# Kernel tuning notes

Measured on AMD Instinct MI355X. Metric: run time of the kernel, lower is better.

Reference implementation:

```python
import jax, jax.numpy as jnp
import numpy as np

TAU = 2.0      # LIF membrane time constant (spikingjelly LIFNode tau=2.0)
V_TH = 1.0     # default spikingjelly threshold
ALPHA = 2.0    # ATan surrogate default alpha

@jax.custom_vjp
def atan_spike(x):
    # Heaviside forward, ATan surrogate backward (spikingjelly surrogate.ATan)
    return (x >= 0.0).astype(x.dtype)

def _spike_fwd(x):
    return atan_spike(x), x

def _spike_bwd(x, g):
    sg = (ALPHA / 2.0) / (1.0 + (jnp.pi / 2.0 * ALPHA * x) ** 2)
    return (g * sg,)

atan_spike.defvjp(_spike_fwd, _spike_bwd)


def setup_inputs() -> dict:
    key = jax.random.key(0)
    ks = jax.random.split(key, 4)
    B, L, C, H, NL, K = 64, 96, 32, 256, 2, 3
    inputs = jax.random.normal(ks[0], (B, L, C), jnp.float32)
    w_enc = jax.random.normal(ks[1], (H, 1, K), jnp.float32) * (1.0 / np.sqrt(K))
    b_enc = jnp.zeros((H,), jnp.float32)
    w_rnn = jax.random.normal(ks[2], (NL, H, H), jnp.float32) * (1.0 / np.sqrt(H))
    b_rnn = jnp.zeros((NL, H), jnp.float32)
    return {"inputs": inputs, "w_enc": w_enc, "b_enc": b_enc,
            "w_rnn": w_rnn, "b_rnn": b_rnn}


def reference(inputs, w_enc, b_enc, w_rnn, b_rnn):
    B, L, C = inputs.shape
    H = w_enc.shape[0]
    NL = w_rnn.shape[0]
    # --- 'conv' spike encoder: per-channel temporal conv -> [B*C, H, L] ---
    x = inputs.transpose(0, 2, 1).reshape(B * C, 1, L)
    h = jax.lax.conv_general_dilated(x, w_enc, (1,), 'SAME',
                                     dimension_numbers=('NCH', 'OIH', 'NCH'))
    h = h + b_enc[None, :, None]
    h = h.transpose(2, 0, 1)  # [L, B*C, H] time-major for scan

    def step(v, x_t):
        s = x_t
        new_v = []
        for l in range(NL):  # fixed small layer loop
            cur = s @ w_rnn[l].T + b_rnn[l]            # Linear
            vl = v[l] + (cur - v[l]) / TAU             # leaky integrate
            s = atan_spike(vl - V_TH)                  # fire (surrogate grad)
            vl = vl * (1.0 - jax.lax.stop_gradient(s)) # hard reset, detach_reset
            new_v.append(vl)
        return tuple(new_v), (s, new_v[-1])

    v0 = tuple(jnp.zeros((B * C, H), inputs.dtype) for _ in range(NL))
    _, (spks, mems) = jax.lax.scan(step, v0, h)
    # spks: [L, B*C, H] -> [B, C*H, L]
    spks = spks.reshape(L, B, C * H).transpose(1, 2, 0)
    return spks.transpose(0, 2, 1), spks[:, :, -1]
```

## Files before the change

### kernel.cpp

```cpp
#include <hip/hip_runtime.h>
#include <hip/hip_bf16.h>
#include <stdint.h>


using floatx4 = __attribute__((ext_vector_type(4))) float;
using intx4   = __attribute__((ext_vector_type(4))) int;

__global__ void prep_kernel(const float* __restrict__ w_enc,
                            const float* __restrict__ b_enc,
                            const float* __restrict__ w_rnn,
                            const float* __restrict__ b_rnn,
                            double* __restrict__ Wd,
                            double* __restrict__ C0d,
                            signed char* __restrict__ Bw8)
{
    const int o = blockIdx.x;
    const int lane = threadIdx.x;
    const float4 w0v = *(const float4*)(w_rnn + (size_t)o * 256 + lane * 4);
    double a0 = 0.0, a1 = 0.0, a2 = 0.0, ab = 0.0;
#pragma unroll
    for (int e = 0; e < 4; ++e) {
        const int i = lane * 4 + e;
        const double wv = (double)(((const float*)&w0v)[e]);
        a0 += wv * (double)w_enc[i * 3 + 0];
        a1 += wv * (double)w_enc[i * 3 + 1];
        a2 += wv * (double)w_enc[i * 3 + 2];
        ab += wv * (double)b_enc[i];
    }
    for (int off = 32; off > 0; off >>= 1) {
        a0 += __shfl_down(a0, off, 64);
        a1 += __shfl_down(a1, off, 64);
        a2 += __shfl_down(a2, off, 64);
        ab += __shfl_down(ab, off, 64);
    }
    if (lane == 0) {
        Wd[o * 3 + 0] = a0;
        Wd[o * 3 + 1] = a1;
        Wd[o * 3 + 2] = a2;
        C0d[o] = ab + (double)b_rnn[o];
    }
    const float4 w1v = *(const float4*)(w_rnn + 65536 + (size_t)o * 256 + lane * 4);
    unsigned int pack[4] = {0u, 0u, 0u, 0u};
#pragma unroll
    for (int e = 0; e < 4; ++e) {
        float f = ((const float*)&w1v)[e];
        int q = __double2int_rn((double)f * 134217728.0);
        int d3 = ((q + 64) & 127) - 64;  q = (q - d3) >> 7;
        int d2 = ((q + 64) & 127) - 64;  q = (q - d2) >> 7;
        int d1 = ((q + 64) & 127) - 64;  q = (q - d1) >> 7;
        int d0 = q;
        pack[0] |= ((unsigned int)(d0 & 0xFF)) << (8 * e);
        pack[1] |= ((unsigned int)(d1 & 0xFF)) << (8 * e);
        pack[2] |= ((unsigned int)(d2 & 0xFF)) << (8 * e);
        pack[3] |= ((unsigned int)(d3 & 0xFF)) << (8 * e);
    }
#pragma unroll
    for (int l = 0; l < 4; ++l)
        *(unsigned int*)(Bw8 + ((size_t)o * 4 + l) * 256 + lane * 4) = pack[l];
}

__global__ void enc_kernel(const float* __restrict__ inputs,
                           const double* __restrict__ Wd,
                           const double* __restrict__ C0d,
                           unsigned char* __restrict__ s0b)
{
    const int n = blockIdx.x;
    const int tidx = threadIdx.x;
    const int b = n >> 5, c = n & 31;
    __shared__ float xr[98];
    if (tidx < 96)       xr[tidx + 1] = inputs[((size_t)b * 96 + tidx) * 32 + c];
    else if (tidx == 96) xr[0]  = 0.0f;
    else if (tidx == 97) xr[97] = 0.0f;
    __syncthreads();
    const double W0 = Wd[tidx * 3], W1 = Wd[tidx * 3 + 1], W2 = Wd[tidx * 3 + 2];
    const double c0 = C0d[tidx];
    const int wid = tidx >> 6, lane = tidx & 63;
    float v = 0.0f;
    for (int t = 0; t < 96; ++t) {
        float cur = (float)((double)xr[t] * W0 + (double)xr[t + 1] * W1 +
                            (double)xr[t + 2] * W2 + c0);
        float vv = v + (cur - v) * 0.5f;
        int sp = (vv - 1.0f) >= 0.0f;
        v = sp ? 0.0f : vv;
        unsigned long long bal = __ballot(sp);
        if ((lane & 15) == 0) {
            const int j = lane >> 4;
            *(unsigned short*)(s0b + ((size_t)t * 2048 + n) * 32 + 8 * j + 2 * wid)
                = (unsigned short)(bal >> (16 * j));
        }
    }
}

__global__ __launch_bounds__(256, 2) void rnn_kernel(
    const unsigned char* __restrict__ s0b,
    const signed char* __restrict__ Bw8,
    const float* __restrict__ b_rnn,
    float* __restrict__ out0,
    float* __restrict__ out1)
{
    const int tid  = threadIdx.x;
    const int wid  = tid >> 6, lane = tid & 63;
    const int m    = lane & 15, g = lane >> 4;
    const int job  = blockIdx.x * 4 + wid;
    const int rt   = job >> 4;
    const int nw   = rt * 16;
    const int o0   = (job & 15) * 16;

    intx4 bfrag[4][4];
#pragma unroll
    for (int l = 0; l < 4; ++l)
#pragma unroll
        for (int c = 0; c < 4; ++c)
            bfrag[l][c] = *(const intx4*)(Bw8 + ((size_t)(o0 + m) * 4 + l) * 256
                                               + c * 64 + g * 16);
    const float bias = b_rnn[256 + o0 + m];

    float* pr[4];
    int    row_r[4];
#pragma unroll
    for (int r = 0; r < 4; ++r) {
        const int row = nw + g * 4 + r;
        row_r[r] = row;
        pr[r] = out0 + ((size_t)(row >> 5) * 96) * 8192 + (size_t)(row & 31) * 256
                     + o0 + m;
    }

    const unsigned char* mp = s0b + ((size_t)(nw + m)) * 32 + 8 * g;
    uint2 m0 = *(const uint2*)(mp);
    uint2 m1 = *(const uint2*)(mp + 65536);

    floatx4 v = {0.f, 0.f, 0.f, 0.f};

    for (int t = 0; t < 96; ++t) {
        uint2 pa = m1;
        if (t < 94)
            m1 = *(const uint2*)(mp + (size_t)(t + 2) * 65536);

        unsigned int hw[4] = { m0.x & 0xFFFFu, m0.x >> 16,
                               m0.y & 0xFFFFu, m0.y >> 16 };
        intx4 af[4];
#pragma unroll
        for (int c = 0; c < 4; ++c) {
            unsigned int h = hw[c];
            intx4 a;
            a.x = (int)((( h        & 0xFu) * 0x00204081u) & 0x01010101u);
            a.y = (int)((((h >> 4)  & 0xFu) * 0x00204081u) & 0x01010101u);
            a.z = (int)((((h >> 8)  & 0xFu) * 0x00204081u) & 0x01010101u);
            a.w = (int)((((h >> 12) & 0xFu) * 0x00204081u) & 0x01010101u);
            af[c] = a;
        }

        intx4 acc0 = {0,0,0,0}, acc1 = {0,0,0,0}, acc2 = {0,0,0,0}, acc3 = {0,0,0,0};
#pragma unroll
        for (int c = 0; c < 4; ++c) {
            acc0 = __builtin_amdgcn_mfma_i32_16x16x64_i8(af[c], bfrag[0][c], acc0, 0, 0, 0);
            acc1 = __builtin_amdgcn_mfma_i32_16x16x64_i8(af[c], bfrag[1][c], acc1, 0, 0, 0);
            acc2 = __builtin_amdgcn_mfma_i32_16x16x64_i8(af[c], bfrag[2][c], acc2, 0, 0, 0);
            acc3 = __builtin_amdgcn_mfma_i32_16x16x64_i8(af[c], bfrag[3][c], acc3, 0, 0, 0);
        }

#pragma unroll
        for (int r = 0; r < 4; ++r) {
            int a01 = acc0[r] * 128 + acc1[r];
            int a23 = acc2[r] * 128 + acc3[r];
            double dd = (double)a01 * 16384.0 + (double)a23;
            float cur = (float)(dd * 7.450580596923828125e-9) + bias;
            float vv = v[r];
            vv = vv + (cur - vv) * 0.5f;
            float s = ((vv - 1.0f) >= 0.0f) ? 1.0f : 0.0f;
            v[r] = vv * (1.0f - s);
            pr[r][(size_t)t * 8192] = s;
            if (t == 95)
                out1[(size_t)row_r[r] * 256 + o0 + m] = s;
        }
        m0 = pa;
    }
}

extern "C" void kernel_launch(void* const* d_in, const int* in_sizes, int n_in,
                              void* d_out, int out_size, void* d_ws, size_t ws_size,
                              hipStream_t stream) {
    const float* inputs = (const float*)d_in[0];
    const float* w_enc  = (const float*)d_in[1];
    const float* b_enc  = (const float*)d_in[2];
    const float* w_rnn  = (const float*)d_in[3];
    const float* b_rnn  = (const float*)d_in[4];

    float* out0 = (float*)d_out;
    float* out1 = out0 + (size_t)64 * 96 * 8192;

    char* ws = (char*)d_ws;
    double*      Wd  = (double*)(ws);
    double*      C0d = (double*)(ws + 6144);
    signed char* Bw8 = (signed char*)(ws + 8192);
    unsigned char* s0b = (unsigned char*)(ws + 270336);

    prep_kernel<<<256, 64, 0, stream>>>(w_enc, b_enc, w_rnn, b_rnn, Wd, C0d, Bw8);
    enc_kernel<<<2048, 256, 0, stream>>>(inputs, Wd, C0d, s0b);
    rnn_kernel<<<512, 256, 0, stream>>>(s0b, Bw8, b_rnn, out0, out1);
}
```

Baseline: 262.2 us.

## Write layer-2 spikes as packed bits and expand to floats in separate kernel

The recurrent kernel no longer scatters strided float stores to the output. It packs each lane's four spikes into a nibble byte in a workspace buffer, and a new expand kernel then writes out0 and out1 as coalesced float4 stores. The MFMA operands are swapped so each lane holds four output rows of one batch row, the double-precision current reconstruction becomes float FMAs, and the guard on the prefetch is dropped by reading past the end of the padded buffer. The change costs an extra kernel launch and an intermediate pass through global memory, and the float reconstruction may round differently near the threshold.

```diff
diff --git a/kernel.cpp b/kernel.cpp
--- a/kernel.cpp
+++ b/kernel.cpp
@@ -95,8 +95,7 @@
     const unsigned char* __restrict__ s0b,
     const signed char* __restrict__ Bw8,
     const float* __restrict__ b_rnn,
-    float* __restrict__ out0,
-    float* __restrict__ out1)
+    unsigned char* __restrict__ s1b)
 {
     const int tid  = threadIdx.x;
     const int wid  = tid >> 6, lane = tid & 63;
@@ -104,7 +103,8 @@
     const int job  = blockIdx.x * 4 + wid;
     const int rt   = job >> 4;
     const int nw   = rt * 16;
-    const int o0   = (job & 15) * 16;
+    const int jo   = job & 15;
+    const int o0   = jo * 16;
 
     intx4 bfrag[4][4];
 #pragma unroll
@@ -113,17 +113,9 @@
         for (int c = 0; c < 4; ++c)
             bfrag[l][c] = *(const intx4*)(Bw8 + ((size_t)(o0 + m) * 4 + l) * 256
                                                + c * 64 + g * 16);
-    const float bias = b_rnn[256 + o0 + m];
-
-    float* pr[4];
-    int    row_r[4];
-#pragma unroll
-    for (int r = 0; r < 4; ++r) {
-        const int row = nw + g * 4 + r;
-        row_r[r] = row;
-        pr[r] = out0 + ((size_t)(row >> 5) * 96) * 8192 + (size_t)(row & 31) * 256
-                     + o0 + m;
-    }
+    const float4 biasv = *(const float4*)(b_rnn + 256 + o0 + g * 4);
+
+    unsigned char* sp_ptr = s1b + (size_t)jo * 8192 + (size_t)(nw + m) * 4 + g;
 
     const unsigned char* mp = s0b + ((size_t)(nw + m)) * 32 + 8 * g;
     uint2 m0 = *(const uint2*)(mp);
@@ -132,48 +124,76 @@
     floatx4 v = {0.f, 0.f, 0.f, 0.f};
 
     for (int t = 0; t < 96; ++t) {
-        uint2 pa = m1;
-        if (t < 94)
-            m1 = *(const uint2*)(mp + (size_t)(t + 2) * 65536);
-
-        unsigned int hw[4] = { m0.x & 0xFFFFu, m0.x >> 16,
-                               m0.y & 0xFFFFu, m0.y >> 16 };
-        intx4 af[4];
-#pragma unroll
-        for (int c = 0; c < 4; ++c) {
-            unsigned int h = hw[c];
-            intx4 a;
-            a.x = (int)((( h        & 0xFu) * 0x00204081u) & 0x01010101u);
-            a.y = (int)((((h >> 4)  & 0xFu) * 0x00204081u) & 0x01010101u);
-            a.z = (int)((((h >> 8)  & 0xFu) * 0x00204081u) & 0x01010101u);
-            a.w = (int)((((h >> 12) & 0xFu) * 0x00204081u) & 0x01010101u);
-            af[c] = a;
-        }
+        uint2 nxt = m1;
+        m1 = *(const uint2*)(mp + (size_t)(t + 2) * 65536);
 
         intx4 acc0 = {0,0,0,0}, acc1 = {0,0,0,0}, acc2 = {0,0,0,0}, acc3 = {0,0,0,0};
-#pragma unroll
-        for (int c = 0; c < 4; ++c) {
-            acc0 = __builtin_amdgcn_mfma_i32_16x16x64_i8(af[c], bfrag[0][c], acc0, 0, 0, 0);
-            acc1 = __builtin_amdgcn_mfma_i32_16x16x64_i8(af[c], bfrag[1][c], acc1, 0, 0, 0);
-            acc2 = __builtin_amdgcn_mfma_i32_16x16x64_i8(af[c], bfrag[2][c], acc2, 0, 0, 0);
-            acc3 = __builtin_amdgcn_mfma_i32_16x16x64_i8(af[c], bfrag[3][c], acc3, 0, 0, 0);
-        }
-
+        {
+            unsigned int hw_[4] = { m0.x & 0xFFFFu, m0.x >> 16,
+                                    m0.y & 0xFFFFu, m0.y >> 16 };
+#pragma unroll
+            for (int c = 0; c < 4; ++c) {
+                unsigned int h_ = hw_[c];
+                intx4 a_;
+                a_.x = (int)((( h_        & 0xFu) * 0x00204081u) & 0x01010101u);
+                a_.y = (int)((((h_ >> 4)  & 0xFu) * 0x00204081u) & 0x01010101u);
+                a_.z = (int)((((h_ >> 8)  & 0xFu) * 0x00204081u) & 0x01010101u);
+                a_.w = (int)((((h_ >> 12) & 0xFu) * 0x00204081u) & 0x01010101u);
+                acc0 = __builtin_amdgcn_mfma_i32_16x16x64_i8(bfrag[0][c], a_, acc0, 0, 0, 0);
+                acc1 = __builtin_amdgcn_mfma_i32_16x16x64_i8(bfrag[1][c], a_, acc1, 0, 0, 0);
+                acc2 = __builtin_amdgcn_mfma_i32_16x16x64_i8(bfrag[2][c], a_, acc2, 0, 0, 0);
+                acc3 = __builtin_amdgcn_mfma_i32_16x16x64_i8(bfrag[3][c], a_, acc3, 0, 0, 0);
+            }
+        }
+
+        unsigned int nib = 0u;
 #pragma unroll
         for (int r = 0; r < 4; ++r) {
             int a01 = acc0[r] * 128 + acc1[r];
             int a23 = acc2[r] * 128 + acc3[r];
-            double dd = (double)a01 * 16384.0 + (double)a23;
-            float cur = (float)(dd * 7.450580596923828125e-9) + bias;
+            float cur = fmaf((float)a01, 0x1p-13f, (float)a23 * 0x1p-27f)
+                        + ((const float*)&biasv)[r];
             float vv = v[r];
             vv = vv + (cur - vv) * 0.5f;
-            float s = ((vv - 1.0f) >= 0.0f) ? 1.0f : 0.0f;
-            v[r] = vv * (1.0f - s);
-            pr[r][(size_t)t * 8192] = s;
-            if (t == 95)
-                out1[(size_t)row_r[r] * 256 + o0 + m] = s;
-        }
-        m0 = pa;
+            bool sp = (vv - 1.0f) >= 0.0f;
+            nib |= sp ? (1u << r) : 0u;
+            v[r] = sp ? 0.0f : vv;
+        }
+        sp_ptr[(size_t)t * 131072] = (unsigned char)nib;
+        m0 = nxt;
+    }
+}
+
+__global__ void expand_kernel(const unsigned char* __restrict__ s1b,
+                              float* __restrict__ out0,
+                              float* __restrict__ out1)
+{
+    const unsigned int tid0 = blockIdx.x * 256u + threadIdx.x;
+#pragma unroll
+    for (int it = 0; it < 6; ++it) {
+        const unsigned int gi = tid0 + (unsigned int)it * 524288u;
+        const unsigned int bt = gi >> 9;
+        const unsigned int b  = bt / 96u;
+        const unsigned int t  = bt - b * 96u;
+        const unsigned int cc = (gi >> 4) & 31u;
+        const unsigned int k  = (gi * 4u) & 63u;
+        const unsigned int n  = b * 32u + cc;
+        const unsigned int quad = *(const unsigned int*)(s1b
+                + (size_t)t * 131072u + (size_t)(k >> 2) * 8192u + (size_t)n * 4u);
+        float* po = out0 + (size_t)gi * 16u;
+        const bool last = (t == 95u);
+        float* p1 = out1 + (size_t)b * 8192u + (size_t)cc * 256u + (size_t)k * 4u;
+#pragma unroll
+        for (int j = 0; j < 4; ++j) {
+            const unsigned int nib = (quad >> (8 * j)) & 0xFu;
+            float4 w;
+            w.x = (float)( nib        & 1u);
+            w.y = (float)((nib >> 1u) & 1u);
+            w.z = (float)((nib >> 2u) & 1u);
+            w.w = (float)((nib >> 3u) & 1u);
+            *(float4*)(po + 4 * j) = w;
+            if (last) *(float4*)(p1 + 4 * j) = w;
+        }
     }
 }
 
@@ -190,12 +210,14 @@
     float* out1 = out0 + (size_t)64 * 96 * 8192;
 
     char* ws = (char*)d_ws;
-    double*      Wd  = (double*)(ws);
-    double*      C0d = (double*)(ws + 6144);
-    signed char* Bw8 = (signed char*)(ws + 8192);
+    double*        Wd  = (double*)(ws);
+    double*        C0d = (double*)(ws + 6144);
+    signed char*   Bw8 = (signed char*)(ws + 8192);
     unsigned char* s0b = (unsigned char*)(ws + 270336);
+    unsigned char* s1b = s0b + (size_t)98 * 65536;
 
     prep_kernel<<<256, 64, 0, stream>>>(w_enc, b_enc, w_rnn, b_rnn, Wd, C0d, Bw8);
     enc_kernel<<<2048, 256, 0, stream>>>(inputs, Wd, C0d, s0b);
-    rnn_kernel<<<512, 256, 0, stream>>>(s0b, Bw8, b_rnn, out0, out1);
-}
+    rnn_kernel<<<512, 256, 0, stream>>>(s0b, Bw8, b_rnn, s1b);
+    expand_kernel<<<2048, 256, 0, stream>>>(s1b, out0, out1);
+}
```

New measurement: 334.7 us. +27.7%, slower.
